# Kernel optimization log

Hardware: AMD Instinct MI355X
Metric: run time of the kernel (lower is better)

Reference implementation:

```python
import jax, jax.numpy as jnp
import numpy as np

B, T, I, H, C = 8192, 784, 1, 30, 10


def setup_inputs() -> dict:
    key = jax.random.key(0)
    ks = jax.random.split(key, 7)
    s_ih = 1.0 / np.sqrt(H)
    return {
        "x": jax.random.normal(ks[0], (B, T, I), dtype=jnp.float32),
        "W_ih": jax.random.uniform(ks[1], (H, I), jnp.float32, -s_ih, s_ih),
        "W_hh": jax.random.uniform(ks[2], (H, H), jnp.float32, -s_ih, s_ih),
        "b_ih": jax.random.uniform(ks[3], (H,), jnp.float32, -s_ih, s_ih),
        "b_hh": jax.random.uniform(ks[4], (H,), jnp.float32, -s_ih, s_ih),
        "W_fc": jax.random.uniform(ks[5], (C, H), jnp.float32, -s_ih, s_ih),
        "b_fc": jax.random.uniform(ks[6], (C,), jnp.float32, -s_ih, s_ih),
    }


def reference(x, W_ih, W_hh, b_ih, b_hh, W_fc, b_fc):
    # x: [B, T, I] -> scan over time. h_t = tanh(x_t W_ih^T + b_ih + h W_hh^T + b_hh)
    xs = jnp.swapaxes(x, 0, 1)  # [T, B, I]
    h0 = jnp.zeros((x.shape[0], W_hh.shape[0]), dtype=x.dtype)
    bias = b_ih + b_hh  # [H]

    def step(h, xt):
        h_new = jnp.tanh(xt @ W_ih.T + h @ W_hh.T + bias)
        return h_new, None

    hT, _ = jax.lax.scan(step, h0, xs)  # hT: [B, H] == out[:, -1, :]
    return hT @ W_fc.T + b_fc  # [B, C]
```

## Files before the change

### kernel.cpp

```cpp
#include <hip/hip_runtime.h>


#define BB 8192
#define TT 784
#define HH 30
#define CC 10

typedef __attribute__((ext_vector_type(8))) short  bf16x8;
typedef __attribute__((ext_vector_type(4))) float  f32x4;
typedef __attribute__((ext_vector_type(4))) unsigned uint4v;

__device__ __forceinline__ float tanh_fast(float a) {
    return 1.0f - 2.0f * __builtin_amdgcn_rcpf(__expf(2.0f * a) + 1.0f);
}

#define BPAIR(p0, p1, hp, lp) do {                                          \
    asm("v_cvt_pk_bf16_f32 %0, %1, %2" : "=v"(hp) : "v"(p0), "v"(p1));      \
    const float _h0 = __uint_as_float((hp) << 16);                          \
    const float _h1 = __uint_as_float((hp) & 0xffff0000u);                  \
    const float _l0 = (p0) - _h0;                                           \
    const float _l1 = (p1) - _h1;                                           \
    asm("v_cvt_pk_bf16_f32 %0, %1, %2" : "=v"(lp) : "v"(_l0), "v"(_l1));    \
} while (0)

__global__ __launch_bounds__(64)
__attribute__((amdgpu_waves_per_eu(1, 1)))
void rnn_scan_kernel(const float* __restrict__ x,
                     const float* __restrict__ W_ih,
                     const float* __restrict__ W_hh,
                     const float* __restrict__ b_ih,
                     const float* __restrict__ b_hh,
                     const float* __restrict__ W_fc,
                     const float* __restrict__ b_fc,
                     float* __restrict__ out) {
    const int lane = threadIdx.x & 63;
    const int n    = lane & 15;
    const int g    = lane >> 4;
    const int b    = blockIdx.x * 16 + n;

    const int r1 = 8 * (n >> 2) + (n & 3);
    const int r2 = r1 + 4;
    unsigned a1h[4], a1l[4], a2h[4], a2l[4];
#pragma unroll
    for (int d = 0; d < 4; ++d) {
        const int k0 = 8 * g + 2 * d, k1 = k0 + 1;
        const float w1a = (k0 < HH) ? W_hh[r1 * HH + k0] : 0.f;
        const float w1b = (k1 < HH) ? W_hh[r1 * HH + k1] : 0.f;
        const float w2a = (r2 < HH && k0 < HH) ? W_hh[r2 * HH + k0] : 0.f;
        const float w2b = (r2 < HH && k1 < HH) ? W_hh[r2 * HH + k1] : 0.f;
        const unsigned u1a = __float_as_uint(w1a), u1b = __float_as_uint(w1b);
        const unsigned u2a = __float_as_uint(w2a), u2b = __float_as_uint(w2b);
        a1h[d] = (u1b & 0xffff0000u) | (u1a >> 16);
        a2h[d] = (u2b & 0xffff0000u) | (u2a >> 16);
        const float l1a = w1a - __uint_as_float(u1a & 0xffff0000u);
        const float l1b = w1b - __uint_as_float(u1b & 0xffff0000u);
        const float l2a = w2a - __uint_as_float(u2a & 0xffff0000u);
        const float l2b = w2b - __uint_as_float(u2b & 0xffff0000u);
        a1l[d] = (__float_as_uint(l1b) & 0xffff0000u) | (__float_as_uint(l1a) >> 16);
        a2l[d] = (__float_as_uint(l2b) & 0xffff0000u) | (__float_as_uint(l2a) >> 16);
    }
    bf16x8 A1h = __builtin_bit_cast(bf16x8, (uint4v){a1h[0], a1h[1], a1h[2], a1h[3]});
    bf16x8 A1l = __builtin_bit_cast(bf16x8, (uint4v){a1l[0], a1l[1], a1l[2], a1l[3]});
    bf16x8 A2h = __builtin_bit_cast(bf16x8, (uint4v){a2h[0], a2h[1], a2h[2], a2h[3]});
    bf16x8 A2l = __builtin_bit_cast(bf16x8, (uint4v){a2l[0], a2l[1], a2l[2], a2l[3]});
    asm volatile("" : "+v"(A1h), "+v"(A1l), "+v"(A2h), "+v"(A2l));

    float bias1[4], wih1[4], bias2[4], wih2[4];
#pragma unroll
    for (int r = 0; r < 4; ++r) {
        const int q1 = 8 * g + r;
        bias1[r] = b_ih[q1] + b_hh[q1];
        wih1[r]  = W_ih[q1];
        const int q2 = q1 + 4;
        bias2[r] = (q2 < HH) ? (b_ih[q2] + b_hh[q2]) : 0.f;
        wih2[r]  = (q2 < HH) ? W_ih[q2] : 0.f;
        asm volatile("" : "+v"(bias1[r]), "+v"(wih1[r]), "+v"(bias2[r]), "+v"(wih2[r]));
    }

    float h0 = 0.f, h1 = 0.f, h2 = 0.f, h3 = 0.f;
    float h4 = 0.f, h5 = 0.f, h6 = 0.f, h7 = 0.f;

    const float* xp = x + (size_t)b * TT;
    float4 xq = *(const float4*)xp;

    for (int qq = 0; qq < TT / 4; ++qq) {
        const float4 nxt = (qq + 1 < TT / 4) ? *(const float4*)(xp + (qq + 1) * 4)
                                             : make_float4(0.f, 0.f, 0.f, 0.f);
#pragma unroll
        for (int u = 0; u < 4; ++u) {
            const float xt = (u == 0) ? xq.x : (u == 1) ? xq.y
                           : (u == 2) ? xq.z : xq.w;
            f32x4 acc1 = { fmaf(xt, wih1[0], bias1[0]), fmaf(xt, wih1[1], bias1[1]),
                           fmaf(xt, wih1[2], bias1[2]), fmaf(xt, wih1[3], bias1[3]) };
            f32x4 acc2 = { fmaf(xt, wih2[0], bias2[0]), fmaf(xt, wih2[1], bias2[1]),
                           fmaf(xt, wih2[2], bias2[2]), fmaf(xt, wih2[3], bias2[3]) };
            unsigned bh0, bh1, bh2, bh3, bl0, bl1, bl2, bl3;
            BPAIR(h0, h1, bh0, bl0);
            BPAIR(h2, h3, bh1, bl1);
            BPAIR(h4, h5, bh2, bl2);
            BPAIR(h6, h7, bh3, bl3);
            const bf16x8 Bh = __builtin_bit_cast(bf16x8, (uint4v){bh0, bh1, bh2, bh3});
            const bf16x8 Bl = __builtin_bit_cast(bf16x8, (uint4v){bl0, bl1, bl2, bl3});
            acc1 = __builtin_amdgcn_mfma_f32_16x16x32_bf16(A1h, Bh, acc1, 0, 0, 0);
            acc2 = __builtin_amdgcn_mfma_f32_16x16x32_bf16(A2h, Bh, acc2, 0, 0, 0);
            acc1 = __builtin_amdgcn_mfma_f32_16x16x32_bf16(A1h, Bl, acc1, 0, 0, 0);
            acc2 = __builtin_amdgcn_mfma_f32_16x16x32_bf16(A2h, Bl, acc2, 0, 0, 0);
            acc1 = __builtin_amdgcn_mfma_f32_16x16x32_bf16(A1l, Bh, acc1, 0, 0, 0);
            acc2 = __builtin_amdgcn_mfma_f32_16x16x32_bf16(A2l, Bh, acc2, 0, 0, 0);
            h0 = tanh_fast(acc1[0]); h1 = tanh_fast(acc1[1]);
            h2 = tanh_fast(acc1[2]); h3 = tanh_fast(acc1[3]);
            h4 = tanh_fast(acc2[0]); h5 = tanh_fast(acc2[1]);
            h6 = tanh_fast(acc2[2]); h7 = tanh_fast(acc2[3]);
        }
        xq = nxt;
    }

    const float hreg[8] = {h0, h1, h2, h3, h4, h5, h6, h7};
#pragma unroll
    for (int c = 0; c < CC; ++c) {
        float p = 0.f;
#pragma unroll
        for (int j = 0; j < 8; ++j) {
            const int k = 8 * g + j;
            if (k < HH) p = fmaf(W_fc[c * HH + k], hreg[j], p);
        }
        p += __shfl_xor(p, 16);
        p += __shfl_xor(p, 32);
        if (g == 0) out[(size_t)b * CC + c] = p + b_fc[c];
    }
}

extern "C" void kernel_launch(void* const* d_in, const int* in_sizes, int n_in,
                              void* d_out, int out_size, void* d_ws, size_t ws_size,
                              hipStream_t stream) {
    const float* x    = (const float*)d_in[0];
    const float* W_ih = (const float*)d_in[1];
    const float* W_hh = (const float*)d_in[2];
    const float* b_ih = (const float*)d_in[3];
    const float* b_hh = (const float*)d_in[4];
    const float* W_fc = (const float*)d_in[5];
    const float* b_fc = (const float*)d_in[6];

    hipLaunchKernelGGL(rnn_scan_kernel,
                       dim3(BB / 16), dim3(64), 0, stream,
                       x, W_ih, W_hh, b_ih, b_hh, W_fc, b_fc,
                       (float*)d_out);
}
```

Baseline: 289.1 us.

## Fold tanh doubling into weights, split MFMA chains, prefetch x two ahead

Pre-scales W_hh, W_ih and the biases by 2 so the tanh no longer multiplies its argument by 2 each step. The three dependent MFMAs per output tile become two independent chains, hi*hi accumulated onto the input term and the two correction products starting from zero, joined by a vector add. This shortens the serial MFMA dependency on the recurrence critical path. The x loads are prefetched two float4 groups ahead instead of one. The cost is an extra add per step and slightly different rounding, since the correction terms are summed separately and the low parts now carry the doubled weights.

```diff
diff --git a/kernel.cpp b/kernel.cpp
--- a/kernel.cpp
+++ b/kernel.cpp
@@ -10,8 +10,8 @@
 typedef __attribute__((ext_vector_type(4))) float  f32x4;
 typedef __attribute__((ext_vector_type(4))) unsigned uint4v;
 
-__device__ __forceinline__ float tanh_fast(float a) {
-    return 1.0f - 2.0f * __builtin_amdgcn_rcpf(__expf(2.0f * a) + 1.0f);
+__device__ __forceinline__ float tanh_pre(float s) {
+    return 1.0f - 2.0f * __builtin_amdgcn_rcpf(__expf(s) + 1.0f);
 }
 
 #define BPAIR(p0, p1, hp, lp) do {                                          \
@@ -44,10 +44,10 @@
 #pragma unroll
     for (int d = 0; d < 4; ++d) {
         const int k0 = 8 * g + 2 * d, k1 = k0 + 1;
-        const float w1a = (k0 < HH) ? W_hh[r1 * HH + k0] : 0.f;
-        const float w1b = (k1 < HH) ? W_hh[r1 * HH + k1] : 0.f;
-        const float w2a = (r2 < HH && k0 < HH) ? W_hh[r2 * HH + k0] : 0.f;
-        const float w2b = (r2 < HH && k1 < HH) ? W_hh[r2 * HH + k1] : 0.f;
+        const float w1a = (k0 < HH) ? 2.0f * W_hh[r1 * HH + k0] : 0.f;
+        const float w1b = (k1 < HH) ? 2.0f * W_hh[r1 * HH + k1] : 0.f;
+        const float w2a = (r2 < HH && k0 < HH) ? 2.0f * W_hh[r2 * HH + k0] : 0.f;
+        const float w2b = (r2 < HH && k1 < HH) ? 2.0f * W_hh[r2 * HH + k1] : 0.f;
         const unsigned u1a = __float_as_uint(w1a), u1b = __float_as_uint(w1b);
         const unsigned u2a = __float_as_uint(w2a), u2b = __float_as_uint(w2b);
         a1h[d] = (u1b & 0xffff0000u) | (u1a >> 16);
@@ -69,11 +69,11 @@
 #pragma unroll
     for (int r = 0; r < 4; ++r) {
         const int q1 = 8 * g + r;
-        bias1[r] = b_ih[q1] + b_hh[q1];
-        wih1[r]  = W_ih[q1];
+        bias1[r] = 2.0f * (b_ih[q1] + b_hh[q1]);
+        wih1[r]  = 2.0f * W_ih[q1];
         const int q2 = q1 + 4;
-        bias2[r] = (q2 < HH) ? (b_ih[q2] + b_hh[q2]) : 0.f;
-        wih2[r]  = (q2 < HH) ? W_ih[q2] : 0.f;
+        bias2[r] = (q2 < HH) ? 2.0f * (b_ih[q2] + b_hh[q2]) : 0.f;
+        wih2[r]  = (q2 < HH) ? 2.0f * W_ih[q2] : 0.f;
         asm volatile("" : "+v"(bias1[r]), "+v"(wih1[r]), "+v"(bias2[r]), "+v"(wih2[r]));
     }
 
@@ -81,19 +81,21 @@
     float h4 = 0.f, h5 = 0.f, h6 = 0.f, h7 = 0.f;
 
     const float* xp = x + (size_t)b * TT;
+    const int NQ = TT / 4;
     float4 xq = *(const float4*)xp;
+    float4 xn = *(const float4*)(xp + 4);
 
-    for (int qq = 0; qq < TT / 4; ++qq) {
-        const float4 nxt = (qq + 1 < TT / 4) ? *(const float4*)(xp + (qq + 1) * 4)
-                                             : make_float4(0.f, 0.f, 0.f, 0.f);
+    for (int qq = 0; qq < NQ; ++qq) {
+        const float4 xf = (qq + 2 < NQ) ? *(const float4*)(xp + (qq + 2) * 4)
+                                        : make_float4(0.f, 0.f, 0.f, 0.f);
 #pragma unroll
         for (int u = 0; u < 4; ++u) {
             const float xt = (u == 0) ? xq.x : (u == 1) ? xq.y
                            : (u == 2) ? xq.z : xq.w;
-            f32x4 acc1 = { fmaf(xt, wih1[0], bias1[0]), fmaf(xt, wih1[1], bias1[1]),
-                           fmaf(xt, wih1[2], bias1[2]), fmaf(xt, wih1[3], bias1[3]) };
-            f32x4 acc2 = { fmaf(xt, wih2[0], bias2[0]), fmaf(xt, wih2[1], bias2[1]),
-                           fmaf(xt, wih2[2], bias2[2]), fmaf(xt, wih2[3], bias2[3]) };
+            f32x4 accP1 = { fmaf(xt, wih1[0], bias1[0]), fmaf(xt, wih1[1], bias1[1]),
+                            fmaf(xt, wih1[2], bias1[2]), fmaf(xt, wih1[3], bias1[3]) };
+            f32x4 accP2 = { fmaf(xt, wih2[0], bias2[0]), fmaf(xt, wih2[1], bias2[1]),
+                            fmaf(xt, wih2[2], bias2[2]), fmaf(xt, wih2[3], bias2[3]) };
             unsigned bh0, bh1, bh2, bh3, bl0, bl1, bl2, bl3;
             BPAIR(h0, h1, bh0, bl0);
             BPAIR(h2, h3, bh1, bl1);
@@ -101,18 +103,22 @@
             BPAIR(h6, h7, bh3, bl3);
             const bf16x8 Bh = __builtin_bit_cast(bf16x8, (uint4v){bh0, bh1, bh2, bh3});
             const bf16x8 Bl = __builtin_bit_cast(bf16x8, (uint4v){bl0, bl1, bl2, bl3});
-            acc1 = __builtin_amdgcn_mfma_f32_16x16x32_bf16(A1h, Bh, acc1, 0, 0, 0);
-            acc2 = __builtin_amdgcn_mfma_f32_16x16x32_bf16(A2h, Bh, acc2, 0, 0, 0);
-            acc1 = __builtin_amdgcn_mfma_f32_16x16x32_bf16(A1h, Bl, acc1, 0, 0, 0);
-            acc2 = __builtin_amdgcn_mfma_f32_16x16x32_bf16(A2h, Bl, acc2, 0, 0, 0);
-            acc1 = __builtin_amdgcn_mfma_f32_16x16x32_bf16(A1l, Bh, acc1, 0, 0, 0);
-            acc2 = __builtin_amdgcn_mfma_f32_16x16x32_bf16(A2l, Bh, acc2, 0, 0, 0);
-            h0 = tanh_fast(acc1[0]); h1 = tanh_fast(acc1[1]);
-            h2 = tanh_fast(acc1[2]); h3 = tanh_fast(acc1[3]);
-            h4 = tanh_fast(acc2[0]); h5 = tanh_fast(acc2[1]);
-            h6 = tanh_fast(acc2[2]); h7 = tanh_fast(acc2[3]);
+            const f32x4 zed = {0.f, 0.f, 0.f, 0.f};
+            accP1 = __builtin_amdgcn_mfma_f32_16x16x32_bf16(A1h, Bh, accP1, 0, 0, 0);
+            accP2 = __builtin_amdgcn_mfma_f32_16x16x32_bf16(A2h, Bh, accP2, 0, 0, 0);
+            f32x4 q1 = __builtin_amdgcn_mfma_f32_16x16x32_bf16(A1h, Bl, zed, 0, 0, 0);
+            f32x4 q2 = __builtin_amdgcn_mfma_f32_16x16x32_bf16(A2h, Bl, zed, 0, 0, 0);
+            q1 = __builtin_amdgcn_mfma_f32_16x16x32_bf16(A1l, Bh, q1, 0, 0, 0);
+            q2 = __builtin_amdgcn_mfma_f32_16x16x32_bf16(A2l, Bh, q2, 0, 0, 0);
+            const f32x4 s1 = accP1 + q1;
+            const f32x4 s2 = accP2 + q2;
+            h0 = tanh_pre(s1[0]); h1 = tanh_pre(s1[1]);
+            h2 = tanh_pre(s1[2]); h3 = tanh_pre(s1[3]);
+            h4 = tanh_pre(s2[0]); h5 = tanh_pre(s2[1]);
+            h6 = tanh_pre(s2[2]); h7 = tanh_pre(s2[3]);
         }
-        xq = nxt;
+        xq = xn;
+        xn = xf;
     }
 
     const float hreg[8] = {h0, h1, h2, h3, h4, h5, h6, h7};
```

New measurement: 287.2 us. No clear change (-0.6%).
